# Kernel tuning notes

Hardware: AMD Instinct MI355X
Metric: run time of the kernel (lower is better)

The kernel has to match this reference:

```python
import jax, jax.numpy as jnp
import numpy as np

N, DEG, F_IN, F_OUT = 50000, 16, 128, 128
E = N * DEG


def setup_inputs() -> dict:
    key = jax.random.key(0)
    k1, k2, k3 = jax.random.split(key, 3)
    x = jax.random.normal(k1, (N, F_IN), dtype=jnp.float32)
    # flat ragged neighbor features: edge e belongs to node seg_ids[e]
    neigh = jax.random.normal(k2, (E, F_IN), dtype=jnp.float32)
    seg_ids = (jnp.arange(E, dtype=jnp.int32) // DEG)  # sorted, each node has DEG neighbors
    # nn.Linear(in, out, bias=False) weight: [out_features, in_features]
    W = jax.random.normal(k3, (F_OUT, F_IN), dtype=jnp.float32) / np.sqrt(F_IN)
    return {"x": x, "neigh": neigh, "seg_ids": seg_ids, "W": W}


def reference(x, neigh, seg_ids, W):
    n = x.shape[0]
    # per-node mean of neighbor features (segment mean over ragged lists)
    ones = jnp.ones((neigh.shape[0],), dtype=x.dtype)
    counts = jax.ops.segment_sum(ones, seg_ids, num_segments=n)  # [N]
    f = jax.ops.segment_sum(neigh, seg_ids, num_segments=n) / counts[:, None]  # [N, F_in]
    # shared linear transform (no bias)
    x_out = (x + f) @ W.T          # [N, F_out]
    neigh_out = neigh @ W.T        # [E, F_out] (all ragged neighbor sets, flat)
    return (x_out, neigh_out)
```

## Files before the change

kernel.cpp:

```cpp
#include <hip/hip_runtime.h>
#include <hip/hip_bf16.h>

#define FDIM  128
#define GNODE 8
#define DEGC  16
#define TROWS 128
#define ROWB  256

typedef __attribute__((ext_vector_type(8))) short   bvec8;
typedef __attribute__((ext_vector_type(8))) __bf16  bf16v8;
typedef __attribute__((ext_vector_type(4))) float   fvec4;

__device__ __forceinline__ fvec4 mfma16(bvec8 a, bvec8 b, fvec4 c) {
    return __builtin_amdgcn_mfma_f32_16x16x32_bf16(
        __builtin_bit_cast(bf16v8, a), __builtin_bit_cast(bf16v8, b), c, 0, 0, 0);
}

__device__ __forceinline__ void st8(char* base, int row, int bir, bvec8 v) {
    *(bvec8*)(base + row * ROWB + (bir ^ ((row & 7) << 4))) = v;
}
__device__ __forceinline__ bvec8 ld8(const char* base, int row, int bir) {
    return *(const bvec8*)(base + row * ROWB + (bir ^ ((row & 7) << 4)));
}

__device__ __forceinline__ bvec8 ldcvt(const float* __restrict__ p) {
    float4 lo = ((const float4*)p)[0], hi = ((const float4*)p)[1];
    bf16v8 o;
    o[0] = (__bf16)lo.x; o[1] = (__bf16)lo.y; o[2] = (__bf16)lo.z; o[3] = (__bf16)lo.w;
    o[4] = (__bf16)hi.x; o[5] = (__bf16)hi.y; o[6] = (__bf16)hi.z; o[7] = (__bf16)hi.w;
    return __builtin_bit_cast(bvec8, o);
}

__device__ __forceinline__ void stage_w(const float* __restrict__ W, char* lds_w, int t) {
    const int sl = t & 15, wr = t >> 4;
    #pragma unroll
    for (int i = 0; i < 8; ++i) {
        const int row = i * 16 + wr;
        st8(lds_w, row, sl * 16, ldcvt(W + (size_t)row * FDIM + sl * 8));
    }
}

__global__ __launch_bounds__(256, 4)
void gcn_main(const float* __restrict__ neigh, const float* __restrict__ W,
              float* __restrict__ out_nb, __hip_bfloat16* __restrict__ nsum_ws)
{
    __shared__ __align__(16) char lds_w[FDIM * ROWB];

    const int t    = threadIdx.x;
    const int blk  = blockIdx.x;
    const int wave = t >> 6, lane = t & 63;
    const int lr = lane & 15, lg = lane >> 4;

    stage_w(W, lds_w, t);
    __syncthreads();

    const float* arow0 = neigh + ((size_t)blk * TROWS + wave * 32 + lr) * FDIM;
    const float* arow1 = arow0 + 16 * FDIM;

    fvec4 acc[2][8];
    #pragma unroll
    for (int i = 0; i < 2; ++i)
        #pragma unroll
        for (int j = 0; j < 8; ++j) acc[i][j] = (fvec4){0.f, 0.f, 0.f, 0.f};

    #pragma unroll
    for (int ks = 0; ks < 4; ++ks) {
        bvec8 a0 = ldcvt(arow0 + ks * 32 + lg * 8);
        bvec8 a1 = ldcvt(arow1 + ks * 32 + lg * 8);
        const int kb = ks * 64 + lg * 16;
        #pragma unroll
        for (int tn = 0; tn < 8; ++tn) {
            bvec8 b = ld8(lds_w, tn * 16 + lr, kb);
            acc[0][tn] = mfma16(a0, b, acc[0][tn]);
            acc[1][tn] = mfma16(a1, b, acc[1][tn]);
        }
    }

    #pragma unroll
    for (int tm = 0; tm < 2; ++tm) {
        const size_t rbase = (size_t)blk * TROWS + wave * 32 + tm * 16 + lg * 4;
        #pragma unroll
        for (int tn = 0; tn < 8; ++tn)
            #pragma unroll
            for (int r = 0; r < 4; ++r)
                out_nb[(rbase + r) * FDIM + tn * 16 + lr] = acc[tm][tn][r];
    }

    #pragma unroll
    for (int tm = 0; tm < 2; ++tm) {
        const int node = blk * GNODE + wave * 2 + tm;
        #pragma unroll
        for (int tn = 0; tn < 8; ++tn) {
            float p = acc[tm][tn][0] + acc[tm][tn][1] + acc[tm][tn][2] + acc[tm][tn][3];
            p += __shfl_xor(p, 16);
            p += __shfl_xor(p, 32);
            if (lg == 0)
                nsum_ws[(size_t)node * FDIM + tn * 16 + lr] =
                    __float2bfloat16(p * (1.f / 16.f));
        }
    }
}

__global__ __launch_bounds__(256, 4)
void gcn_xout(const float* __restrict__ x, const float* __restrict__ W,
              const __hip_bfloat16* __restrict__ nsum_ws,
              float* __restrict__ out_x, int n)
{
    __shared__ __align__(16) char lds_w[FDIM * ROWB];

    const int t    = threadIdx.x;
    const int blk  = blockIdx.x;
    const int wave = t >> 6, lane = t & 63;
    const int lr = lane & 15, lg = lane >> 4;

    stage_w(W, lds_w, t);
    __syncthreads();

    int m0 = blk * TROWS + wave * 32 + lr;
    int m1 = m0 + 16;
    if (m0 > n - 1) m0 = n - 1;
    if (m1 > n - 1) m1 = n - 1;
    const float* arow0 = x + (size_t)m0 * FDIM;
    const float* arow1 = x + (size_t)m1 * FDIM;

    fvec4 acc[2][8];
    #pragma unroll
    for (int i = 0; i < 2; ++i)
        #pragma unroll
        for (int j = 0; j < 8; ++j) acc[i][j] = (fvec4){0.f, 0.f, 0.f, 0.f};

    #pragma unroll
    for (int ks = 0; ks < 4; ++ks) {
        bvec8 a0 = ldcvt(arow0 + ks * 32 + lg * 8);
        bvec8 a1 = ldcvt(arow1 + ks * 32 + lg * 8);
        const int kb = ks * 64 + lg * 16;
        #pragma unroll
        for (int tn = 0; tn < 8; ++tn) {
            bvec8 b = ld8(lds_w, tn * 16 + lr, kb);
            acc[0][tn] = mfma16(a0, b, acc[0][tn]);
            acc[1][tn] = mfma16(a1, b, acc[1][tn]);
        }
    }

    #pragma unroll
    for (int tm = 0; tm < 2; ++tm) {
        const size_t rbase = (size_t)blk * TROWS + wave * 32 + tm * 16 + lg * 4;
        #pragma unroll
        for (int tn = 0; tn < 8; ++tn)
            #pragma unroll
            for (int r = 0; r < 4; ++r) {
                const size_t m = rbase + r;
                if ((int)m < n) {
                    const size_t idx = m * FDIM + tn * 16 + lr;
                    out_x[idx] = acc[tm][tn][r] + __bfloat162float(nsum_ws[idx]);
                }
            }
    }
}

extern "C" void kernel_launch(void* const* d_in, const int* in_sizes, int n_in,
                              void* d_out, int out_size, void* d_ws, size_t ws_size,
                              hipStream_t stream) {
    const float* x     = (const float*)d_in[0];
    const float* neigh = (const float*)d_in[1];
    const float* W     = (const float*)d_in[3];

    const int n = in_sizes[0] / FDIM;
    float* out_x  = (float*)d_out;
    float* out_nb = out_x + (size_t)n * FDIM;
    __hip_bfloat16* nsum = (__hip_bfloat16*)d_ws;

    const int blocks1 = n / GNODE;
    hipLaunchKernelGGL(gcn_main, dim3(blocks1), dim3(256), 0, stream,
                       neigh, W, out_nb, nsum);

    const int blocks2 = (n + TROWS - 1) / TROWS;
    hipLaunchKernelGGL(gcn_xout, dim3(blocks2), dim3(256), 0, stream,
                       x, W, nsum, out_x, n);
}
```

Measured before the change: 206.1 us.

## Fuse x_out GEMM into neighbor kernel, keeping node means in LDS

Merges the two kernels into one. Each block now also computes its 8 nodes' x@W.T with small MFMA tiles and adds the neighbor mean held in shared memory. This drops the bf16 workspace round trip, the second launch and the second W staging. In exchange each block does extra MFMA work that runs at low utilisation (8 valid rows in a 16-row tile), adds a second __syncthreads, and uses more LDS per block, which may affect occupancy.

```diff
diff --git a/kernel.cpp b/kernel.cpp
--- a/kernel.cpp
+++ b/kernel.cpp
@@ -41,10 +41,12 @@
 }
 
 __global__ __launch_bounds__(256, 4)
-void gcn_main(const float* __restrict__ neigh, const float* __restrict__ W,
-              float* __restrict__ out_nb, __hip_bfloat16* __restrict__ nsum_ws)
+void gcn_fused(const float* __restrict__ x, const float* __restrict__ neigh,
+               const float* __restrict__ W,
+               float* __restrict__ out_x, float* __restrict__ out_nb)
 {
-    __shared__ __align__(16) char lds_w[FDIM * ROWB];
+    __shared__ __align__(16) char  lds_w[FDIM * ROWB];
+    __shared__            float nsum[GNODE][FDIM];
 
     const int t    = threadIdx.x;
     const int blk  = blockIdx.x;
@@ -88,72 +90,42 @@
 
     #pragma unroll
     for (int tm = 0; tm < 2; ++tm) {
-        const int node = blk * GNODE + wave * 2 + tm;
+        const int node = wave * 2 + tm;
         #pragma unroll
         for (int tn = 0; tn < 8; ++tn) {
             float p = acc[tm][tn][0] + acc[tm][tn][1] + acc[tm][tn][2] + acc[tm][tn][3];
             p += __shfl_xor(p, 16);
             p += __shfl_xor(p, 32);
-            if (lg == 0)
-                nsum_ws[(size_t)node * FDIM + tn * 16 + lr] =
-                    __float2bfloat16(p * (1.f / 16.f));
-        }
-    }
-}
-
-__global__ __launch_bounds__(256, 4)
-void gcn_xout(const float* __restrict__ x, const float* __restrict__ W,
-              const __hip_bfloat16* __restrict__ nsum_ws,
-              float* __restrict__ out_x, int n)
-{
-    __shared__ __align__(16) char lds_w[FDIM * ROWB];
-
-    const int t    = threadIdx.x;
-    const int blk  = blockIdx.x;
-    const int wave = t >> 6, lane = t & 63;
-    const int lr = lane & 15, lg = lane >> 4;
-
-    stage_w(W, lds_w, t);
-    __syncthreads();
-
-    int m0 = blk * TROWS + wave * 32 + lr;
-    int m1 = m0 + 16;
-    if (m0 > n - 1) m0 = n - 1;
-    if (m1 > n - 1) m1 = n - 1;
-    const float* arow0 = x + (size_t)m0 * FDIM;
-    const float* arow1 = x + (size_t)m1 * FDIM;
-
-    fvec4 acc[2][8];
-    #pragma unroll
-    for (int i = 0; i < 2; ++i)
-        #pragma unroll
-        for (int j = 0; j < 8; ++j) acc[i][j] = (fvec4){0.f, 0.f, 0.f, 0.f};
-
-    #pragma unroll
-    for (int ks = 0; ks < 4; ++ks) {
-        bvec8 a0 = ldcvt(arow0 + ks * 32 + lg * 8);
-        bvec8 a1 = ldcvt(arow1 + ks * 32 + lg * 8);
-        const int kb = ks * 64 + lg * 16;
-        #pragma unroll
-        for (int tn = 0; tn < 8; ++tn) {
-            bvec8 b = ld8(lds_w, tn * 16 + lr, kb);
-            acc[0][tn] = mfma16(a0, b, acc[0][tn]);
-            acc[1][tn] = mfma16(a1, b, acc[1][tn]);
+            if (lg == 0) nsum[node][tn * 16 + lr] = p * (1.f / 16.f);
         }
     }
 
+    const float* xrow = x + ((size_t)(blk * GNODE) + (lr & 7)) * FDIM;
+    fvec4 accx[2];
+    accx[0] = (fvec4){0.f, 0.f, 0.f, 0.f};
+    accx[1] = (fvec4){0.f, 0.f, 0.f, 0.f};
     #pragma unroll
-    for (int tm = 0; tm < 2; ++tm) {
-        const size_t rbase = (size_t)blk * TROWS + wave * 32 + tm * 16 + lg * 4;
+    for (int ks = 0; ks < 4; ++ks) {
+        bvec8 ax = ldcvt(xrow + ks * 32 + lg * 8);
+        const int kb = ks * 64 + lg * 16;
         #pragma unroll
-        for (int tn = 0; tn < 8; ++tn)
+        for (int j = 0; j < 2; ++j) {
+            bvec8 b = ld8(lds_w, (wave * 2 + j) * 16 + lr, kb);
+            accx[j] = mfma16(ax, b, accx[j]);
+        }
+    }
+
+    __syncthreads();
+
+    if (lg < 2) {
+        #pragma unroll
+        for (int j = 0; j < 2; ++j)
             #pragma unroll
             for (int r = 0; r < 4; ++r) {
-                const size_t m = rbase + r;
-                if ((int)m < n) {
-                    const size_t idx = m * FDIM + tn * 16 + lr;
-                    out_x[idx] = acc[tm][tn][r] + __bfloat162float(nsum_ws[idx]);
-                }
+                const int node = lg * 4 + r;
+                const int feat = (wave * 2 + j) * 16 + lr;
+                out_x[((size_t)blk * GNODE + node) * FDIM + feat] =
+                    accx[j][r] + nsum[node][feat];
             }
     }
 }
@@ -168,13 +140,8 @@
     const int n = in_sizes[0] / FDIM;
     float* out_x  = (float*)d_out;
     float* out_nb = out_x + (size_t)n * FDIM;
-    __hip_bfloat16* nsum = (__hip_bfloat16*)d_ws;
 
-    const int blocks1 = n / GNODE;
-    hipLaunchKernelGGL(gcn_main, dim3(blocks1), dim3(256), 0, stream,
-                       neigh, W, out_nb, nsum);
-
-    const int blocks2 = (n + TROWS - 1) / TROWS;
-    hipLaunchKernelGGL(gcn_xout, dim3(blocks2), dim3(256), 0, stream,
-                       x, W, nsum, out_x, n);
+    const int blocks = n / GNODE;
+    hipLaunchKernelGGL(gcn_fused, dim3(blocks), dim3(256), 0, stream,
+                       x, neigh, W, out_x, out_nb);
 }
```

Result: faster. 190.1 us (-7.7%).
